# Kernel optimization log

Hardware: AMD Instinct MI355X
Metric: run time of the kernel (lower is better)

Reference implementation:

```python
import jax, jax.numpy as jnp
import numpy as np

COMMITMENT_COST = 0.25


def setup_inputs() -> dict:
    key = jax.random.key(0)
    k1, k2 = jax.random.split(key)
    B, S, D, K = 16, 4096, 256, 4096
    inputs = jax.random.normal(k1, (B, S, D), dtype=jnp.float32)
    # codebook ~ embedding.weight (init scale irrelevant for correctness baseline)
    codebook = jax.random.normal(k2, (K, D), dtype=jnp.float32)
    return {"inputs": inputs, "codebook": codebook}


def reference(inputs, codebook):
    B, S, D = inputs.shape
    flat = inputs.reshape(-1, D)  # (N, D)
    distances = (
        jnp.sum(flat * flat, axis=1, keepdims=True)
        + jnp.sum(codebook * codebook, axis=1)
        - 2.0 * jnp.matmul(flat, codebook.T)
    )
    encoding_indices = jnp.argmin(distances, axis=1)  # (N,)
    quantized = codebook[encoding_indices].reshape(inputs.shape)  # gather
    # commitment loss: beta * mse(inputs, sg(quantized))
    diff = inputs - jax.lax.stop_gradient(quantized)
    commitment_loss = COMMITMENT_COST * jnp.mean(diff * diff)
    # straight-through estimator
    quantized_st = inputs + jax.lax.stop_gradient(quantized - inputs)
    return quantized_st, commitment_loss, encoding_indices
```

## Files before the change

kernel.cpp:

```cpp
#include <hip/hip_runtime.h>
#include <hip/hip_bf16.h>
#include <stdint.h>

typedef _Float16 half8 __attribute__((ext_vector_type(8)));
typedef float f32x4 __attribute__((ext_vector_type(4)));

#define DDIM 256
#define KCODES 4096
#define BM 128
#define BN 256
#define NTILES (KCODES / BN)
#define NCHUNK (DDIM / 64)
#define DELTA 0.02f
#define FLT_BIG 3.4e38f

__global__ void cvt_cb_kernel(const float* __restrict__ cb, half8* __restrict__ cb16) {
    int gid = blockIdx.x * 256 + threadIdx.x;
    int slot = gid & 15;
    int chunk = (gid >> 4) & 3;
    int code = gid >> 6;
    int g = slot >> 3, part = (slot >> 2) & 1, quad = slot & 3;
    int d0 = chunk * 64 + g * 32 + quad * 8;
    const float* src = &cb[(size_t)code * DDIM + d0];
    half8 h;
    #pragma unroll
    for (int j = 0; j < 8; ++j) {
        float v = src[j];
        _Float16 hi = (_Float16)v;
        h[j] = part ? (_Float16)(v - (float)hi) : hi;
    }
    cb16[gid] = h;
}

__global__ void enorm_kernel(const float* __restrict__ cb, float* __restrict__ en, int K) {
    int gid = blockIdx.x * blockDim.x + threadIdx.x;
    int code = gid >> 6;
    int lane = threadIdx.x & 63;
    if (code >= K) return;
    const float4 v = *reinterpret_cast<const float4*>(&cb[(size_t)code * DDIM + lane * 4]);
    float s = v.x * v.x + v.y * v.y + v.z * v.z + v.w * v.w;
    #pragma unroll
    for (int off = 32; off > 0; off >>= 1) s += __shfl_xor(s, off, 64);
    if (lane == 0) en[code] = s;
}

__global__ __launch_bounds__(512, 2)
void vq_mfma_kernel(const float* __restrict__ x, const half8* __restrict__ cb16,
                    const float* __restrict__ en, int* __restrict__ bidx_out,
                    int* __restrict__ list, int* __restrict__ counter) {
    __shared__ __align__(16) _Float16 Asl[BM * 128];
    __shared__ __align__(16) _Float16 Bsl[BN * 128];
    __shared__ float red_d[4][BM];
    __shared__ float red_d2[4][BM];
    __shared__ int   red_i[4][BM];

    const int tid = threadIdx.x;
    const int lane = tid & 63;
    const int w = tid >> 6;
    const int wr = w >> 2, wc = w & 3;
    const int l15 = lane & 15, l4 = lane >> 4;
    const int brow = blockIdx.x * BM;

    float best[16], best2[16];
    int bid[16];
    #pragma unroll
    for (int i = 0; i < 16; ++i) { best[i] = FLT_BIG; best2[i] = FLT_BIG; bid[i] = 0; }

    const int arow = tid >> 2;
    const int aq = tid & 3;
    const float* axp = &x[(size_t)(brow + arow) * DDIM + aq * 16];
    half8* Ap = (half8*)Asl;
    half8* Bp = (half8*)Bsl;
    const int aswz = arow & 7;
    const int abase = arow * 16;
    const int ah0 = (aq >> 1) * 8 + (aq & 1) * 2;

    for (int ct = 0; ct < NTILES; ++ct) {
        const int c0 = ct * BN;
        f32x4 acc[4][4];
        #pragma unroll
        for (int m = 0; m < 4; ++m)
            #pragma unroll
            for (int n = 0; n < 4; ++n) acc[m][n] = (f32x4){0.f, 0.f, 0.f, 0.f};

        for (int c = 0; c < NCHUNK; ++c) {
            __syncthreads();
            {
                const float4* ax4 = (const float4*)(axp + c * 64);
                float4 f0 = ax4[0], f1 = ax4[1], f2 = ax4[2], f3 = ax4[3];
                float vv[16] = {f0.x, f0.y, f0.z, f0.w, f1.x, f1.y, f1.z, f1.w,
                                f2.x, f2.y, f2.z, f2.w, f3.x, f3.y, f3.z, f3.w};
                half8 hv0, hv1, lv0, lv1;
                #pragma unroll
                for (int j = 0; j < 8; ++j) {
                    _Float16 h = (_Float16)vv[j];
                    hv0[j] = h; lv0[j] = (_Float16)(vv[j] - (float)h);
                }
                #pragma unroll
                for (int j = 0; j < 8; ++j) {
                    _Float16 h = (_Float16)vv[8 + j];
                    hv1[j] = h; lv1[j] = (_Float16)(vv[8 + j] - (float)h);
                }
                Ap[abase + ((ah0    ) ^ aswz)] = hv0;
                Ap[abase + ((ah0 + 1) ^ aswz)] = hv1;
                Ap[abase + ((ah0 + 4) ^ aswz)] = lv0;
                Ap[abase + ((ah0 + 5) ^ aswz)] = lv1;
            }
            #pragma unroll
            for (int i = 0; i < 8; ++i) {
                int S = i * 512 + tid;
                int r = S >> 4, l = S & 15;
                half8 v = cb16[((size_t)(c0 + r) * NCHUNK + c) * 16 + l];
                Bp[r * 16 + (l ^ (r & 7))] = v;
            }
            __syncthreads();

            #pragma unroll
            for (int g = 0; g < 2; ++g) {
                half8 ah[4], al[4], bh[4], bl[4];
                #pragma unroll
                for (int m = 0; m < 4; ++m) {
                    int row = wr * 64 + m * 16 + l15;
                    int sw = row & 7;
                    int sh = g * 8 + l4;
                    ah[m] = Ap[row * 16 + ((sh    ) ^ sw)];
                    al[m] = Ap[row * 16 + ((sh + 4) ^ sw)];
                }
                #pragma unroll
                for (int n = 0; n < 4; ++n) {
                    int col = wc * 64 + n * 16 + l15;
                    int sw = col & 7;
                    int sh = g * 8 + l4;
                    bh[n] = Bp[col * 16 + ((sh    ) ^ sw)];
                    bl[n] = Bp[col * 16 + ((sh + 4) ^ sw)];
                }
                #pragma unroll
                for (int m = 0; m < 4; ++m)
                    #pragma unroll
                    for (int n = 0; n < 4; ++n) {
                        acc[m][n] = __builtin_amdgcn_mfma_f32_16x16x32_f16(ah[m], bh[n], acc[m][n], 0, 0, 0);
                        acc[m][n] = __builtin_amdgcn_mfma_f32_16x16x32_f16(al[m], bh[n], acc[m][n], 0, 0, 0);
                        acc[m][n] = __builtin_amdgcn_mfma_f32_16x16x32_f16(ah[m], bl[n], acc[m][n], 0, 0, 0);
                    }
            }
        }

        #pragma unroll
        for (int n = 0; n < 4; ++n) {
            int code = c0 + wc * 64 + n * 16 + l15;
            float e = en[code];
            #pragma unroll
            for (int m = 0; m < 4; ++m) {
                #pragma unroll
                for (int r = 0; r < 4; ++r) {
                    float dist = fmaf(-2.f, acc[m][n][r], e);
                    int ri = m * 4 + r;
                    if (dist < best[ri]) {
                        best2[ri] = best[ri]; best[ri] = dist; bid[ri] = code;
                    } else if (dist < best2[ri]) {
                        best2[ri] = dist;
                    }
                }
            }
        }
    }

    #pragma unroll
    for (int ri = 0; ri < 16; ++ri) {
        float d = best[ri], d2 = best2[ri];
        int ix = bid[ri];
        #pragma unroll
        for (int off = 1; off < 16; off <<= 1) {
            float od = __shfl_xor(d, off, 64);
            float od2 = __shfl_xor(d2, off, 64);
            int oi = __shfl_xor(ix, off, 64);
            if (od < d || (od == d && oi < ix)) {
                d2 = fminf(d, od2); d = od; ix = oi;
            } else {
                d2 = fminf(d2, od);
            }
        }
        if (l15 == 0) {
            int row = wr * 64 + (ri >> 2) * 16 + l4 * 4 + (ri & 3);
            red_d[wc][row] = d;
            red_d2[wc][row] = d2;
            red_i[wc][row] = ix;
        }
    }
    __syncthreads();

    if (tid < BM) {
        float d = red_d[0][tid], d2 = red_d2[0][tid];
        int ix = red_i[0][tid];
        #pragma unroll
        for (int q = 1; q < 4; ++q) {
            float od = red_d[q][tid], od2 = red_d2[q][tid];
            int oi = red_i[q][tid];
            if (od < d || (od == d && oi < ix)) {
                d2 = fminf(d, od2); d = od; ix = oi;
            } else {
                d2 = fminf(d2, od);
            }
        }
        bidx_out[brow + tid] = ix;
        if (d2 - d < DELTA) {
            int pos = atomicAdd(counter, 1);
            list[pos] = brow + tid;
        }
    }
}

__global__ __launch_bounds__(256)
void rescan_kernel(const float* __restrict__ x, const float* __restrict__ cb,
                   const float* __restrict__ en, const int* __restrict__ list,
                   const int* __restrict__ counter, int* __restrict__ bidx) {
    __shared__ __align__(16) float4 xrow4[64];
    __shared__ float wd[4];
    __shared__ int wi[4];
    const int tid = threadIdx.x;
    const int w = tid >> 6;
    const int lane = tid & 63;
    const int cnt = *counter;

    for (int it = blockIdx.x; it < cnt; it += gridDim.x) {
        const int row = list[it];
        __syncthreads();
        if (tid < 64) xrow4[tid] = ((const float4*)&x[(size_t)row * DDIM])[tid];
        __syncthreads();
        const float4 xv = xrow4[lane];
        float bd = FLT_BIG;
        int bi = 0;
        for (int i = 0; i < KCODES / 4; ++i) {
            int code = i * 4 + w;
            const float4 c4 = ((const float4*)&cb[(size_t)code * DDIM])[lane];
            float s = xv.x * c4.x + xv.y * c4.y + xv.z * c4.z + xv.w * c4.w;
            #pragma unroll
            for (int off = 1; off < 64; off <<= 1) s += __shfl_xor(s, off, 64);
            float dist = fmaf(-2.f, s, en[code]);
            if (dist < bd) { bd = dist; bi = code; }
        }
        if (lane == 0) { wd[w] = bd; wi[w] = bi; }
        __syncthreads();
        if (tid == 0) {
            float d = wd[0]; int ix = wi[0];
            #pragma unroll
            for (int q = 1; q < 4; ++q) {
                if (wd[q] < d || (wd[q] == d && wi[q] < ix)) { d = wd[q]; ix = wi[q]; }
            }
            bidx[row] = ix;
        }
    }
}

__global__ void gather_kernel(const float* __restrict__ x, const float* __restrict__ cb,
                              const int* __restrict__ bidx, float* __restrict__ out,
                              float* __restrict__ loss_accum, int N) {
    __shared__ float wsum[4];
    const int tid = threadIdx.x;
    const int brow = blockIdx.x * BM;
    const size_t ND = (size_t)N * DDIM;
    if (tid < BM) out[ND + 1 + brow + tid] = (float)bidx[brow + tid];
    float lsum = 0.f;
    #pragma unroll 4
    for (int p = 0; p < 32; ++p) {
        int i = tid + p * 256;
        int row = i >> 6;
        int c4 = (i & 63) << 2;
        int code = bidx[brow + row];
        const float4 q = *reinterpret_cast<const float4*>(&cb[(size_t)code * DDIM + c4]);
        const float4 xv = *reinterpret_cast<const float4*>(&x[(size_t)(brow + row) * DDIM + c4]);
        float d0 = xv.x - q.x, d1 = xv.y - q.y, d2 = xv.z - q.z, d3 = xv.w - q.w;
        lsum += d0 * d0 + d1 * d1 + d2 * d2 + d3 * d3;
        *reinterpret_cast<float4*>(&out[(size_t)(brow + row) * DDIM + c4]) = q;
    }
    #pragma unroll
    for (int off = 32; off > 0; off >>= 1) lsum += __shfl_xor(lsum, off, 64);
    if ((tid & 63) == 0) wsum[tid >> 6] = lsum;
    __syncthreads();
    if (tid == 0) {
        float tot = wsum[0] + wsum[1] + wsum[2] + wsum[3];
        atomicAdd(loss_accum, tot * (0.25f / (float)ND));
    }
}

__global__ void loss_fin_kernel(const float* __restrict__ loss_accum,
                                float* __restrict__ out, size_t off) {
    if (blockIdx.x == 0 && threadIdx.x == 0) out[off] = *loss_accum;
}

extern "C" void kernel_launch(void* const* d_in, const int* in_sizes, int n_in,
                              void* d_out, int out_size, void* d_ws, size_t ws_size,
                              hipStream_t stream) {
    const float* x = (const float*)d_in[0];
    const float* cb = (const float*)d_in[1];
    const int N = in_sizes[0] / DDIM;
    const int K = in_sizes[1] / DDIM;
    float* out = (float*)d_out;

    half8* cb16 = (half8*)d_ws;
    char* p = (char*)d_ws + (4 << 20);
    float* en = (float*)p;                  p += (size_t)K * 4;
    int* bidx = (int*)p;                    p += (size_t)N * 4;
    int* list = (int*)p;                    p += (size_t)N * 4;
    int* counter = (int*)p;                 p += 64;
    float* loss_accum = (float*)p;

    hipMemsetAsync(counter, 0, sizeof(int), stream);
    hipMemsetAsync(loss_accum, 0, sizeof(float), stream);
    cvt_cb_kernel<<<(K * 64) / 256, 256, 0, stream>>>(cb, cb16);
    enorm_kernel<<<(K * 64) / 256, 256, 0, stream>>>(cb, en, K);
    vq_mfma_kernel<<<N / BM, 512, 0, stream>>>(x, cb16, en, bidx, list, counter);
    rescan_kernel<<<512, 256, 0, stream>>>(x, cb, en, list, counter, bidx);
    gather_kernel<<<N / BM, 256, 0, stream>>>(x, cb, bidx, out, loss_accum, N);
    loss_fin_kernel<<<1, 64, 0, stream>>>(loss_accum, out, (size_t)N * DDIM);
}
```

Before: 781.0 us.

## Pre-split inputs to fp16 hi/lo and double-buffer tiles via direct global-to-LDS loads

Adds a pre-pass that converts x into a hi/lo fp16 layout stored in the output buffer, so the main kernel no longer converts activations inside its loop. The main GEMM loop becomes a flat double-buffered pipeline over 32-wide K chunks, using global_load_lds to stream A and B tiles straight into shared memory while the MFMAs run on the other buffer. Codebook norms are cached in LDS and MFMA sections get raised wave priority. This adds an extra full pass over x, reuses the output buffer as scratch, and relies on hand-placed waitcnt and barrier ordering.

```diff
diff --git a/kernel.cpp b/kernel.cpp
--- a/kernel.cpp
+++ b/kernel.cpp
@@ -9,27 +9,32 @@
 #define KCODES 4096
 #define BM 128
 #define BN 256
-#define NTILES (KCODES / BN)
-#define NCHUNK (DDIM / 64)
+#define NCH 8
+#define TILES (KCODES / BN)
+#define STEPS (TILES * NCH)
 #define DELTA 0.02f
 #define FLT_BIG 3.4e38f
 
-__global__ void cvt_cb_kernel(const float* __restrict__ cb, half8* __restrict__ cb16) {
+#define GLOAD_LDS(gsrc, ldst)                                                        \
+    __builtin_amdgcn_global_load_lds(                                                \
+        (const __attribute__((address_space(1))) void*)(const void*)(gsrc),          \
+        (__attribute__((address_space(3))) void*)(void*)(ldst), 16, 0, 0)
+
+__global__ void cvt_hl_kernel(const float* __restrict__ src, half8* __restrict__ dst) {
     int gid = blockIdx.x * 256 + threadIdx.x;
-    int slot = gid & 15;
-    int chunk = (gid >> 4) & 3;
-    int code = gid >> 6;
-    int g = slot >> 3, part = (slot >> 2) & 1, quad = slot & 3;
-    int d0 = chunk * 64 + g * 32 + quad * 8;
-    const float* src = &cb[(size_t)code * DDIM + d0];
+    int p = gid & 7;
+    int ch = (gid >> 3) & 7;
+    long row = gid >> 6;
+    int part = p >> 2, quad = p & 3;
+    const float* s = src + row * DDIM + ch * 32 + quad * 8;
     half8 h;
     #pragma unroll
     for (int j = 0; j < 8; ++j) {
-        float v = src[j];
+        float v = s[j];
         _Float16 hi = (_Float16)v;
         h[j] = part ? (_Float16)(v - (float)hi) : hi;
     }
-    cb16[gid] = h;
+    dst[gid] = h;
 }
 
 __global__ void enorm_kernel(const float* __restrict__ cb, float* __restrict__ en, int K) {
@@ -44,12 +49,35 @@
     if (lane == 0) en[code] = s;
 }
 
+__device__ __forceinline__ void stage_step(int st, int w, int lane, int brow,
+                                           const half8* __restrict__ x16,
+                                           const half8* __restrict__ cb16,
+                                           half8* Ab, half8* Bb) {
+    const int ct = st >> 3, ch = st & 7;
+    #pragma unroll
+    for (int i = 0; i < 6; ++i) {
+        const int r = w * 6 + i;
+        if (r < 16) {
+            int sl = r * 64 + lane;
+            int row = sl >> 3, p = sl & 7;
+            const half8* src = x16 + ((size_t)(brow + row) * NCH + ch) * 8 + (p ^ (row & 7));
+            GLOAD_LDS(src, Ab + r * 64);
+        } else {
+            int sl = (r - 16) * 64 + lane;
+            int row = sl >> 3, p = sl & 7;
+            const half8* src = cb16 + ((size_t)(ct * BN + row) * NCH + ch) * 8 + (p ^ (row & 7));
+            GLOAD_LDS(src, Bb + (r - 16) * 64);
+        }
+    }
+}
+
 __global__ __launch_bounds__(512, 2)
-void vq_mfma_kernel(const float* __restrict__ x, const half8* __restrict__ cb16,
+void vq_mfma_kernel(const half8* __restrict__ x16, const half8* __restrict__ cb16,
                     const float* __restrict__ en, int* __restrict__ bidx_out,
                     int* __restrict__ list, int* __restrict__ counter) {
-    __shared__ __align__(16) _Float16 Asl[BM * 128];
-    __shared__ __align__(16) _Float16 Bsl[BN * 128];
+    __shared__ __align__(16) half8 Abuf[2][BM * 8];
+    __shared__ __align__(16) half8 Bbuf[2][BN * 8];
+    __shared__ float en_lds[KCODES];
     __shared__ float red_d[4][BM];
     __shared__ float red_d2[4][BM];
     __shared__ int   red_i[4][BM];
@@ -61,108 +89,88 @@
     const int l15 = lane & 15, l4 = lane >> 4;
     const int brow = blockIdx.x * BM;
 
+    for (int i = tid; i < KCODES; i += 512) en_lds[i] = en[i];
+
+    stage_step(0, w, lane, brow, x16, cb16, Abuf[0], Bbuf[0]);
+    stage_step(1, w, lane, brow, x16, cb16, Abuf[1], Bbuf[1]);
+    __syncthreads();
+
     float best[16], best2[16];
     int bid[16];
     #pragma unroll
     for (int i = 0; i < 16; ++i) { best[i] = FLT_BIG; best2[i] = FLT_BIG; bid[i] = 0; }
 
-    const int arow = tid >> 2;
-    const int aq = tid & 3;
-    const float* axp = &x[(size_t)(brow + arow) * DDIM + aq * 16];
-    half8* Ap = (half8*)Asl;
-    half8* Bp = (half8*)Bsl;
-    const int aswz = arow & 7;
-    const int abase = arow * 16;
-    const int ah0 = (aq >> 1) * 8 + (aq & 1) * 2;
-
-    for (int ct = 0; ct < NTILES; ++ct) {
-        const int c0 = ct * BN;
-        f32x4 acc[4][4];
+    f32x4 acc[4][4];
+
+    #pragma unroll 2
+    for (int s = 0; s < STEPS; ++s) {
+        const int b = s & 1;
+        if ((s & 7) == 0) {
+            #pragma unroll
+            for (int m = 0; m < 4; ++m)
+                #pragma unroll
+                for (int n = 0; n < 4; ++n) acc[m][n] = (f32x4){0.f, 0.f, 0.f, 0.f};
+        }
+        const half8* Ap = Abuf[b];
+        const half8* Bp = Bbuf[b];
+        half8 ah[4], al[4], bh[4], bl[4];
+        #pragma unroll
+        for (int m = 0; m < 4; ++m) {
+            int row = wr * 64 + m * 16 + l15;
+            int base = row * 8, sw = row & 7;
+            ah[m] = Ap[base + (l4 ^ sw)];
+            al[m] = Ap[base + ((4 + l4) ^ sw)];
+        }
+        #pragma unroll
+        for (int n = 0; n < 4; ++n) {
+            int col = wc * 64 + n * 16 + l15;
+            int base = col * 8, sw = col & 7;
+            bh[n] = Bp[base + (l4 ^ sw)];
+            bl[n] = Bp[base + ((4 + l4) ^ sw)];
+        }
+        asm volatile("s_waitcnt lgkmcnt(0)" ::: "memory");
+        __builtin_amdgcn_sched_barrier(0);
+        __builtin_amdgcn_s_barrier();
+
+        const bool more = (s + 2 < STEPS);
+        if (more) stage_step(s + 2, w, lane, brow, x16, cb16, Abuf[b], Bbuf[b]);
+
+        __builtin_amdgcn_s_setprio(1);
         #pragma unroll
         for (int m = 0; m < 4; ++m)
             #pragma unroll
-            for (int n = 0; n < 4; ++n) acc[m][n] = (f32x4){0.f, 0.f, 0.f, 0.f};
-
-        for (int c = 0; c < NCHUNK; ++c) {
-            __syncthreads();
-            {
-                const float4* ax4 = (const float4*)(axp + c * 64);
-                float4 f0 = ax4[0], f1 = ax4[1], f2 = ax4[2], f3 = ax4[3];
-                float vv[16] = {f0.x, f0.y, f0.z, f0.w, f1.x, f1.y, f1.z, f1.w,
-                                f2.x, f2.y, f2.z, f2.w, f3.x, f3.y, f3.z, f3.w};
-                half8 hv0, hv1, lv0, lv1;
-                #pragma unroll
-                for (int j = 0; j < 8; ++j) {
-                    _Float16 h = (_Float16)vv[j];
-                    hv0[j] = h; lv0[j] = (_Float16)(vv[j] - (float)h);
-                }
-                #pragma unroll
-                for (int j = 0; j < 8; ++j) {
-                    _Float16 h = (_Float16)vv[8 + j];
-                    hv1[j] = h; lv1[j] = (_Float16)(vv[8 + j] - (float)h);
-                }
-                Ap[abase + ((ah0    ) ^ aswz)] = hv0;
-                Ap[abase + ((ah0 + 1) ^ aswz)] = hv1;
-                Ap[abase + ((ah0 + 4) ^ aswz)] = lv0;
-                Ap[abase + ((ah0 + 5) ^ aswz)] = lv1;
-            }
-            #pragma unroll
-            for (int i = 0; i < 8; ++i) {
-                int S = i * 512 + tid;
-                int r = S >> 4, l = S & 15;
-                half8 v = cb16[((size_t)(c0 + r) * NCHUNK + c) * 16 + l];
-                Bp[r * 16 + (l ^ (r & 7))] = v;
-            }
-            __syncthreads();
-
-            #pragma unroll
-            for (int g = 0; g < 2; ++g) {
-                half8 ah[4], al[4], bh[4], bl[4];
+            for (int n = 0; n < 4; ++n) {
+                acc[m][n] = __builtin_amdgcn_mfma_f32_16x16x32_f16(ah[m], bh[n], acc[m][n], 0, 0, 0);
+                acc[m][n] = __builtin_amdgcn_mfma_f32_16x16x32_f16(al[m], bh[n], acc[m][n], 0, 0, 0);
+                acc[m][n] = __builtin_amdgcn_mfma_f32_16x16x32_f16(ah[m], bl[n], acc[m][n], 0, 0, 0);
+            }
+        __builtin_amdgcn_s_setprio(0);
+
+        if ((s & 7) == 7) {
+            const int c0 = (s >> 3) * BN;
+            #pragma unroll
+            for (int n = 0; n < 4; ++n) {
+                int code = c0 + wc * 64 + n * 16 + l15;
+                float e = en_lds[code];
                 #pragma unroll
                 for (int m = 0; m < 4; ++m) {
-                    int row = wr * 64 + m * 16 + l15;
-                    int sw = row & 7;
-                    int sh = g * 8 + l4;
-                    ah[m] = Ap[row * 16 + ((sh    ) ^ sw)];
-                    al[m] = Ap[row * 16 + ((sh + 4) ^ sw)];
-                }
-                #pragma unroll
-                for (int n = 0; n < 4; ++n) {
-                    int col = wc * 64 + n * 16 + l15;
-                    int sw = col & 7;
-                    int sh = g * 8 + l4;
-                    bh[n] = Bp[col * 16 + ((sh    ) ^ sw)];
-                    bl[n] = Bp[col * 16 + ((sh + 4) ^ sw)];
-                }
-                #pragma unroll
-                for (int m = 0; m < 4; ++m)
                     #pragma unroll
-                    for (int n = 0; n < 4; ++n) {
-                        acc[m][n] = __builtin_amdgcn_mfma_f32_16x16x32_f16(ah[m], bh[n], acc[m][n], 0, 0, 0);
-                        acc[m][n] = __builtin_amdgcn_mfma_f32_16x16x32_f16(al[m], bh[n], acc[m][n], 0, 0, 0);
-                        acc[m][n] = __builtin_amdgcn_mfma_f32_16x16x32_f16(ah[m], bl[n], acc[m][n], 0, 0, 0);
-                    }
-            }
-        }
-
-        #pragma unroll
-        for (int n = 0; n < 4; ++n) {
-            int code = c0 + wc * 64 + n * 16 + l15;
-            float e = en[code];
-            #pragma unroll
-            for (int m = 0; m < 4; ++m) {
-                #pragma unroll
-                for (int r = 0; r < 4; ++r) {
-                    float dist = fmaf(-2.f, acc[m][n][r], e);
-                    int ri = m * 4 + r;
-                    if (dist < best[ri]) {
-                        best2[ri] = best[ri]; best[ri] = dist; bid[ri] = code;
-                    } else if (dist < best2[ri]) {
-                        best2[ri] = dist;
+                    for (int r = 0; r < 4; ++r) {
+                        float dist = fmaf(-2.f, acc[m][n][r], e);
+                        int ri = m * 4 + r;
+                        if (dist < best[ri]) {
+                            best2[ri] = best[ri]; best[ri] = dist; bid[ri] = code;
+                        } else if (dist < best2[ri]) {
+                            best2[ri] = dist;
+                        }
                     }
                 }
             }
         }
+
+        if (more) { asm volatile("s_waitcnt vmcnt(6)" ::: "memory"); }
+        else      { asm volatile("s_waitcnt vmcnt(0)" ::: "memory"); }
+        __builtin_amdgcn_s_barrier();
     }
 
     #pragma unroll
@@ -297,6 +305,8 @@
     const int K = in_sizes[1] / DDIM;
     float* out = (float*)d_out;
 
+    half8* x16 = (half8*)d_out;
+
     half8* cb16 = (half8*)d_ws;
     char* p = (char*)d_ws + (4 << 20);
     float* en = (float*)p;                  p += (size_t)K * 4;
@@ -307,9 +317,10 @@
 
     hipMemsetAsync(counter, 0, sizeof(int), stream);
     hipMemsetAsync(loss_accum, 0, sizeof(float), stream);
-    cvt_cb_kernel<<<(K * 64) / 256, 256, 0, stream>>>(cb, cb16);
+    cvt_hl_kernel<<<(N * 64) / 256, 256, 0, stream>>>(x, x16);
+    cvt_hl_kernel<<<(K * 64) / 256, 256, 0, stream>>>(cb, cb16);
     enorm_kernel<<<(K * 64) / 256, 256, 0, stream>>>(cb, en, K);
-    vq_mfma_kernel<<<N / BM, 512, 0, stream>>>(x, cb16, en, bidx, list, counter);
+    vq_mfma_kernel<<<N / BM, 512, 0, stream>>>(x16, cb16, en, bidx, list, counter);
     rescan_kernel<<<512, 256, 0, stream>>>(x, cb, en, list, counter, bidx);
     gather_kernel<<<N / BM, 256, 0, stream>>>(x, cb, bidx, out, loss_accum, N);
     loss_fin_kernel<<<1, 64, 0, stream>>>(loss_accum, out, (size_t)N * DDIM);
```

Measured after the change: 956.4 us. +22.5%, slower.
